# Optimization experiments

Hardware: AMD Instinct MI355X
Metric: run time of the kernel (lower is better)

Reference implementation:

```python
import jax, jax.numpy as jnp
import numpy as np

N_NODES = 50000
N_EDGES = 800000
N_GRAPHS = 64
IN_DIM, HID, OUT = 128, 128, 16


def gcn_conv(x, src, dst, deg_inv_sqrt, W, b):
    # x: [N, Cin]; src/dst: [E+N] (self-loops appended); W: [Cin, Cout]
    h = x @ W                                   # [N, Cout]
    norm = deg_inv_sqrt[src] * deg_inv_sqrt[dst]  # [E+N]
    msg = h[src] * norm[:, None]                # gather + scale
    out = jax.ops.segment_sum(msg, dst, num_segments=N_NODES)
    return out + b


def setup_inputs() -> dict:
    key = jax.random.key(0)
    ks = jax.random.split(key, 8)
    x = jax.random.normal(ks[0], (N_NODES, IN_DIM), dtype=jnp.float32)
    edge_index = jax.random.randint(ks[1], (2, N_EDGES), 0, N_NODES, dtype=jnp.int64)
    batch = jnp.sort(jax.random.randint(ks[2], (N_NODES,), 0, N_GRAPHS, dtype=jnp.int64))
    s = 1.0 / np.sqrt(IN_DIM)
    W1 = jax.random.normal(ks[3], (IN_DIM, HID), dtype=jnp.float32) * s
    b1 = jnp.zeros((HID,), dtype=jnp.float32)
    W2 = jax.random.normal(ks[4], (HID, HID), dtype=jnp.float32) * (1.0 / np.sqrt(HID))
    b2 = jnp.zeros((HID,), dtype=jnp.float32)
    Wfc = jax.random.normal(ks[5], (HID, OUT), dtype=jnp.float32) * (1.0 / np.sqrt(HID))
    bfc = jnp.zeros((OUT,), dtype=jnp.float32)
    return {"x": x, "edge_index": edge_index, "batch": batch,
            "W1": W1, "b1": b1, "W2": W2, "b2": b2, "Wfc": Wfc, "bfc": bfc}


def reference(x, edge_index, batch, W1, b1, W2, b2, Wfc, bfc):
    self_loops = jnp.arange(N_NODES, dtype=edge_index.dtype)
    src = jnp.concatenate([edge_index[0], self_loops])  # [E+N]
    dst = jnp.concatenate([edge_index[1], self_loops])
    deg = jax.ops.segment_sum(jnp.ones_like(dst, dtype=x.dtype), dst, num_segments=N_NODES)
    deg_inv_sqrt = jnp.where(deg > 0, jax.lax.rsqrt(deg), 0.0)

    h = jax.nn.relu(gcn_conv(x, src, dst, deg_inv_sqrt, W1, b1))
    h = jax.nn.relu(gcn_conv(h, src, dst, deg_inv_sqrt, W2, b2))

    # global mean pool over graphs
    sums = jax.ops.segment_sum(h, batch, num_segments=N_GRAPHS)         # [G, HID]
    cnts = jax.ops.segment_sum(jnp.ones((N_NODES,), h.dtype), batch, num_segments=N_GRAPHS)
    pooled = sums / jnp.maximum(cnts, 1.0)[:, None]

    return pooled @ Wfc + bfc  # [G, OUT]
```

## Files before the change

kernel.cpp:

```cpp
#include <hip/hip_runtime.h>
#include <math.h>

#define N_NODES 50000
#define N_EDGES 800000
#define N_GRAPHS 64
#define DIM 128
#define OUTD 16
#define POOL_BLOCKS 1024

#define BSHIFT 8
#define BNODES 256
#define NBUCK ((N_NODES + BNODES - 1) / BNODES)
#define TILE 2048
#define RCAP 8192
#define BSLOT 4864

typedef __attribute__((ext_vector_type(8))) short short8;
typedef __attribute__((ext_vector_type(4))) float f32x4;

static __device__ __forceinline__ unsigned short f2bf(float f) {
    unsigned u = __float_as_uint(f);
    u += 0x7fffu + ((u >> 16) & 1u);
    return (unsigned short)(u >> 16);
}
static __device__ __forceinline__ float bfl(unsigned u) {
    return __uint_as_float(u << 16);
}
static __device__ __forceinline__ float bfh(unsigned u) {
    return __uint_as_float(u & 0xffff0000u);
}
static __device__ __forceinline__ float b2f(unsigned short u) {
    return __uint_as_float((unsigned)u << 16);
}

__global__ __launch_bounds__(256) void k_init(int* __restrict__ cursor,
                                              float* __restrict__ pool,
                                              float* __restrict__ pcnt) {
    int tid = threadIdx.x;
    if (tid < NBUCK) cursor[tid] = tid * BSLOT;
    for (int i = tid; i < N_GRAPHS * DIM; i += 256) pool[i] = 0.f;
    if (tid < N_GRAPHS) pcnt[tid] = 0.f;
}

__global__ __launch_bounds__(256) void k_binA(const int* __restrict__ src,
                                              const int* __restrict__ dstp,
                                              int* __restrict__ bucket_cursor,
                                              unsigned* __restrict__ bucket_arr) {
    __shared__ int cnt[NBUCK];
    __shared__ int base[NBUCK];
    int tile0 = blockIdx.x * TILE;
    for (int i = threadIdx.x; i < NBUCK; i += 256) cnt[i] = 0;
    __syncthreads();
#pragma unroll
    for (int j = 0; j < TILE / 512; ++j) {
        int e = tile0 + j * 512 + threadIdx.x * 2;
        if (e < N_EDGES) {
            int2 d = *(const int2*)(dstp + e);
            atomicAdd(&cnt[d.x >> BSHIFT], 1);
            atomicAdd(&cnt[d.y >> BSHIFT], 1);
        }
    }
    __syncthreads();
    for (int i = threadIdx.x; i < NBUCK; i += 256) {
        int c = cnt[i];
        base[i] = c ? atomicAdd(&bucket_cursor[i], c) : 0;
        cnt[i] = 0;
    }
    __syncthreads();
#pragma unroll
    for (int j = 0; j < TILE / 512; ++j) {
        int e = tile0 + j * 512 + threadIdx.x * 2;
        if (e < N_EDGES) {
            int2 s = *(const int2*)(src + e);
            int2 d = *(const int2*)(dstp + e);
            int b0 = d.x >> BSHIFT, b1 = d.y >> BSHIFT;
            int p0 = base[b0] + atomicAdd(&cnt[b0], 1);
            bucket_arr[p0] = (unsigned)s.x | ((unsigned)(d.x & 255) << 16);
            int p1 = base[b1] + atomicAdd(&cnt[b1], 1);
            bucket_arr[p1] = (unsigned)s.y | ((unsigned)(d.y & 255) << 16);
        }
    }
}

__global__ __launch_bounds__(256) void k_bases(const int* __restrict__ cursor,
                                               int* __restrict__ base) {
    __shared__ int s[256];
    int tid = threadIdx.x;
    int v = (tid < NBUCK) ? (cursor[tid] - tid * BSLOT) : 0;
    s[tid] = v;
    __syncthreads();
    for (int off = 1; off < 256; off <<= 1) {
        int t = (tid >= off) ? s[tid - off] : 0;
        __syncthreads();
        s[tid] += t;
        __syncthreads();
    }
    if (tid <= NBUCK) base[tid] = s[tid] - v;
}

__global__ __launch_bounds__(256) void k_binB(const unsigned* __restrict__ barr,
                                              const int* __restrict__ base,
                                              int* __restrict__ row_off,
                                              float* __restrict__ dis,
                                              unsigned short* __restrict__ csr) {
    __shared__ unsigned raw[RCAP];
    __shared__ unsigned short stage[RCAP];
    __shared__ int hist[BNODES];
    __shared__ int scn[BNODES];
    int tid = threadIdx.x;
    int b = blockIdx.x;
    int n0 = b << BSHIFT;
    int rbase = base[b];
    int len = base[b + 1] - rbase;
    const unsigned* bin = barr + (size_t)b * BSLOT;

    hist[tid] = 0;
    __syncthreads();
    for (int i = tid; i < len; i += 256) {
        unsigned ed = bin[i];
        if (i < RCAP) raw[i] = ed;
        atomicAdd(&hist[ed >> 16], 1);
    }
    __syncthreads();
    int v = hist[tid];
    scn[tid] = v;
    __syncthreads();
    for (int off = 1; off < 256; off <<= 1) {
        int t = (tid >= off) ? scn[tid - off] : 0;
        __syncthreads();
        scn[tid] += t;
        __syncthreads();
    }
    int excl = scn[tid] - v;
    int n = n0 + tid;
    if (n < N_NODES) {
        row_off[n] = rbase + excl;
        dis[n] = rsqrtf((float)(v + 1));
    }
    if (b == NBUCK - 1 && tid == 0) row_off[N_NODES] = N_EDGES;
    hist[tid] = excl;
    __syncthreads();
    for (int i = tid; i < len; i += 256) {
        unsigned ed = (i < RCAP) ? raw[i] : bin[i];
        int p = atomicAdd(&hist[ed >> 16], 1);
        unsigned short sv = (unsigned short)(ed & 0xffffu);
        if (p < RCAP) stage[p] = sv;
        else csr[rbase + p] = sv;
    }
    __syncthreads();
    int lim = min(len, RCAP);
    for (int i = tid; i < lim; i += 256)
        csr[rbase + i] = stage[i];
}

template <int BF16IN>
__global__ __launch_bounds__(256) void k_gemm(const void* __restrict__ Av,
                                              const float* __restrict__ Wg,
                                              unsigned short* __restrict__ C,
                                              int nrows) {
    __shared__ unsigned smemW[32768 / 4];
    __shared__ unsigned smemC[34816 / 4];
    unsigned* Wl = smemW;
    {
        int t = threadIdx.x;
        int p = t & 63;
        int kp = p * 2;
        int n0 = (t >> 6) * 32;
        int kstep = kp >> 5;
        int quad = (kp >> 3) & 3;
        int jw = (kp & 7) >> 1;
        const float* r0 = Wg + (size_t)kp * DIM;
        const float* r1 = r0 + DIM;
        int rot = (p >> 2) & 7;
#pragma unroll
        for (int i4 = 0; i4 < 8; ++i4) {
            int nb = ((i4 + rot) & 7) * 4;
            int n = n0 + nb;
            float4 lo = *(const float4*)(r0 + n);
            float4 hi = *(const float4*)(r1 + n);
            const float* lp = &lo.x;
            const float* hp = &hi.x;
#pragma unroll
            for (int ii = 0; ii < 4; ++ii) {
                int nn = n + ii;
                int ct = nn >> 4;
                int l  = quad * 16 + (nn & 15);
                unsigned vlo = f2bf(lp[ii]);
                unsigned vhi = f2bf(hp[ii]);
                Wl[(((kstep * 8 + ct) * 64) + l) * 4 + jw] = vlo | (vhi << 16);
            }
        }
    }
    __syncthreads();

    int wid  = threadIdx.x >> 6;
    int lane = threadIdx.x & 63;
    int m    = lane & 15;
    int quad = lane >> 4;
    const short8* Wf = (const short8*)Wl;
    unsigned short* cs = (unsigned short*)smemC + wid * 4352;
    const unsigned char* cb = (const unsigned char*)smemC + wid * 8704;

    int ntiles = (nrows + 127) / 128;
    for (int tile = blockIdx.x; tile < ntiles; tile += gridDim.x) {
        int row0 = tile * 128 + wid * 32;
        if (row0 >= nrows) continue;

        int rA = row0 + m;      if (rA >= nrows) rA = nrows - 1;
        int rB = row0 + 16 + m; if (rB >= nrows) rB = nrows - 1;

        short8 af0[4], af1[4];
        if (BF16IN) {
            const unsigned short* arowA = (const unsigned short*)Av + (size_t)rA * DIM + quad * 8;
            const unsigned short* arowB = (const unsigned short*)Av + (size_t)rB * DIM + quad * 8;
#pragma unroll
            for (int ks = 0; ks < 4; ++ks) {
                af0[ks] = *(const short8*)(arowA + ks * 32);
                af1[ks] = *(const short8*)(arowB + ks * 32);
            }
        } else {
            const float* arowA = (const float*)Av + (size_t)rA * DIM + quad * 8;
            const float* arowB = (const float*)Av + (size_t)rB * DIM + quad * 8;
#pragma unroll
            for (int ks = 0; ks < 4; ++ks) {
                float4 lo = *(const float4*)(arowA + ks * 32);
                float4 hi = *(const float4*)(arowA + ks * 32 + 4);
                short8 f;
                f[0] = (short)f2bf(lo.x); f[1] = (short)f2bf(lo.y);
                f[2] = (short)f2bf(lo.z); f[3] = (short)f2bf(lo.w);
                f[4] = (short)f2bf(hi.x); f[5] = (short)f2bf(hi.y);
                f[6] = (short)f2bf(hi.z); f[7] = (short)f2bf(hi.w);
                af0[ks] = f;
                lo = *(const float4*)(arowB + ks * 32);
                hi = *(const float4*)(arowB + ks * 32 + 4);
                f[0] = (short)f2bf(lo.x); f[1] = (short)f2bf(lo.y);
                f[2] = (short)f2bf(lo.z); f[3] = (short)f2bf(lo.w);
                f[4] = (short)f2bf(hi.x); f[5] = (short)f2bf(hi.y);
                f[6] = (short)f2bf(hi.z); f[7] = (short)f2bf(hi.w);
                af1[ks] = f;
            }
        }

        f32x4 acc0[8], acc1[8];
#pragma unroll
        for (int ct = 0; ct < 8; ++ct) {
            acc0[ct] = (f32x4){0.f, 0.f, 0.f, 0.f};
            acc1[ct] = (f32x4){0.f, 0.f, 0.f, 0.f};
        }

#pragma unroll
        for (int ks = 0; ks < 4; ++ks) {
#pragma unroll
            for (int ct = 0; ct < 8; ++ct) {
                short8 bfrag = Wf[(ks * 8 + ct) * 64 + lane];
                acc0[ct] = __builtin_amdgcn_mfma_f32_16x16x32_bf16(af0[ks], bfrag, acc0[ct], 0, 0, 0);
                acc1[ct] = __builtin_amdgcn_mfma_f32_16x16x32_bf16(af1[ks], bfrag, acc1[ct], 0, 0, 0);
            }
        }

#pragma unroll
        for (int ct = 0; ct < 8; ++ct) {
#pragma unroll
            for (int reg = 0; reg < 4; ++reg) {
                cs[(quad * 4 + reg) * 136 + ct * 16 + m]      = f2bf(acc0[ct][reg]);
                cs[(16 + quad * 4 + reg) * 136 + ct * 16 + m] = f2bf(acc1[ct][reg]);
            }
        }
#pragma unroll
        for (int i = 0; i < 8; ++i) {
            int rg = i * 4 + quad;
            int r = row0 + rg;
            if (r < nrows) {
                uint4 vv = *(const uint4*)(cb + rg * 272 + m * 16);
                *((uint4*)(C + (size_t)r * DIM) + m) = vv;
            }
        }
    }
}

__global__ __launch_bounds__(256) void k_agg(const uint4* __restrict__ Hb4,
                                             const int* __restrict__ row_off,
                                             const unsigned short* __restrict__ csr,
                                             const float* __restrict__ dis,
                                             const float* __restrict__ bias,
                                             uint4* __restrict__ out) {
    int lane = threadIdx.x & 15;
    int node = blockIdx.x * 16 + (threadIdx.x >> 4);
    if (node >= N_NODES) return;

    float dn = dis[node];
    float wself = dn * dn;
    uint4 hp = Hb4[(size_t)node * 16 + lane];
    float a0[8], a1[8], a2[8], a3[8];
    a0[0] = wself * bfl(hp.x); a0[1] = wself * bfh(hp.x);
    a0[2] = wself * bfl(hp.y); a0[3] = wself * bfh(hp.y);
    a0[4] = wself * bfl(hp.z); a0[5] = wself * bfh(hp.z);
    a0[6] = wself * bfl(hp.w); a0[7] = wself * bfh(hp.w);
#pragma unroll
    for (int j = 0; j < 8; ++j) { a1[j] = 0.f; a2[j] = 0.f; a3[j] = 0.f; }

    int e = row_off[node], e1 = row_off[node + 1];
    for (; e + 4 <= e1; e += 4) {
        int s0 = csr[e];     int s1 = csr[e + 1];
        int s2 = csr[e + 2]; int s3 = csr[e + 3];
        uint4 g0 = Hb4[(size_t)s0 * 16 + lane];
        uint4 g1 = Hb4[(size_t)s1 * 16 + lane];
        uint4 g2 = Hb4[(size_t)s2 * 16 + lane];
        uint4 g3 = Hb4[(size_t)s3 * 16 + lane];
        float w0 = dn * dis[s0], w1 = dn * dis[s1];
        float w2 = dn * dis[s2], w3 = dn * dis[s3];
        a0[0] = fmaf(w0, bfl(g0.x), a0[0]); a0[1] = fmaf(w0, bfh(g0.x), a0[1]);
        a0[2] = fmaf(w0, bfl(g0.y), a0[2]); a0[3] = fmaf(w0, bfh(g0.y), a0[3]);
        a0[4] = fmaf(w0, bfl(g0.z), a0[4]); a0[5] = fmaf(w0, bfh(g0.z), a0[5]);
        a0[6] = fmaf(w0, bfl(g0.w), a0[6]); a0[7] = fmaf(w0, bfh(g0.w), a0[7]);
        a1[0] = fmaf(w1, bfl(g1.x), a1[0]); a1[1] = fmaf(w1, bfh(g1.x), a1[1]);
        a1[2] = fmaf(w1, bfl(g1.y), a1[2]); a1[3] = fmaf(w1, bfh(g1.y), a1[3]);
        a1[4] = fmaf(w1, bfl(g1.z), a1[4]); a1[5] = fmaf(w1, bfh(g1.z), a1[5]);
        a1[6] = fmaf(w1, bfl(g1.w), a1[6]); a1[7] = fmaf(w1, bfh(g1.w), a1[7]);
        a2[0] = fmaf(w2, bfl(g2.x), a2[0]); a2[1] = fmaf(w2, bfh(g2.x), a2[1]);
        a2[2] = fmaf(w2, bfl(g2.y), a2[2]); a2[3] = fmaf(w2, bfh(g2.y), a2[3]);
        a2[4] = fmaf(w2, bfl(g2.z), a2[4]); a2[5] = fmaf(w2, bfh(g2.z), a2[5]);
        a2[6] = fmaf(w2, bfl(g2.w), a2[6]); a2[7] = fmaf(w2, bfh(g2.w), a2[7]);
        a3[0] = fmaf(w3, bfl(g3.x), a3[0]); a3[1] = fmaf(w3, bfh(g3.x), a3[1]);
        a3[2] = fmaf(w3, bfl(g3.y), a3[2]); a3[3] = fmaf(w3, bfh(g3.y), a3[3]);
        a3[4] = fmaf(w3, bfl(g3.z), a3[4]); a3[5] = fmaf(w3, bfh(g3.z), a3[5]);
        a3[6] = fmaf(w3, bfl(g3.w), a3[6]); a3[7] = fmaf(w3, bfh(g3.w), a3[7]);
    }
    for (; e < e1; ++e) {
        int s = csr[e];
        uint4 g = Hb4[(size_t)s * 16 + lane];
        float w = dn * dis[s];
        a0[0] = fmaf(w, bfl(g.x), a0[0]); a0[1] = fmaf(w, bfh(g.x), a0[1]);
        a0[2] = fmaf(w, bfl(g.y), a0[2]); a0[3] = fmaf(w, bfh(g.y), a0[3]);
        a0[4] = fmaf(w, bfl(g.z), a0[4]); a0[5] = fmaf(w, bfh(g.z), a0[5]);
        a0[6] = fmaf(w, bfl(g.w), a0[6]); a0[7] = fmaf(w, bfh(g.w), a0[7]);
    }

    float4 b0 = ((const float4*)bias)[lane * 2];
    float4 b1v = ((const float4*)bias)[lane * 2 + 1];
    float r[8];
    r[0] = fmaxf(a0[0] + a1[0] + a2[0] + a3[0] + b0.x, 0.f);
    r[1] = fmaxf(a0[1] + a1[1] + a2[1] + a3[1] + b0.y, 0.f);
    r[2] = fmaxf(a0[2] + a1[2] + a2[2] + a3[2] + b0.z, 0.f);
    r[3] = fmaxf(a0[3] + a1[3] + a2[3] + a3[3] + b0.w, 0.f);
    r[4] = fmaxf(a0[4] + a1[4] + a2[4] + a3[4] + b1v.x, 0.f);
    r[5] = fmaxf(a0[5] + a1[5] + a2[5] + a3[5] + b1v.y, 0.f);
    r[6] = fmaxf(a0[6] + a1[6] + a2[6] + a3[6] + b1v.z, 0.f);
    r[7] = fmaxf(a0[7] + a1[7] + a2[7] + a3[7] + b1v.w, 0.f);
    uint4 ov;
    ov.x = (unsigned)f2bf(r[0]) | ((unsigned)f2bf(r[1]) << 16);
    ov.y = (unsigned)f2bf(r[2]) | ((unsigned)f2bf(r[3]) << 16);
    ov.z = (unsigned)f2bf(r[4]) | ((unsigned)f2bf(r[5]) << 16);
    ov.w = (unsigned)f2bf(r[6]) | ((unsigned)f2bf(r[7]) << 16);
    out[(size_t)node * 16 + lane] = ov;
}

__global__ __launch_bounds__(128) void k_pool(const unsigned short* __restrict__ h,
                                              const int* __restrict__ batch,
                                              float* __restrict__ pool,
                                              float* __restrict__ pcnt) {
    int chunk = (N_NODES + POOL_BLOCKS - 1) / POOL_BLOCKS;
    int n0 = blockIdx.x * chunk;
    int n1 = min(n0 + chunk, N_NODES);
    if (n0 >= n1) return;
    int c = threadIdx.x;
    int curg = batch[n0];
    float acc = 0.f;
    int count = 0;
    int n = n0;
    for (; n + 4 <= n1; ) {
        int g0 = batch[n], g3 = batch[n + 3];
        if (g0 == curg && g3 == curg) {
            float v0 = b2f(h[(size_t)(n + 0) * DIM + c]);
            float v1 = b2f(h[(size_t)(n + 1) * DIM + c]);
            float v2 = b2f(h[(size_t)(n + 2) * DIM + c]);
            float v3 = b2f(h[(size_t)(n + 3) * DIM + c]);
            acc += (v0 + v1) + (v2 + v3);
            count += 4;
            n += 4;
        } else {
            int g = g0;
            if (g != curg) {
                atomicAdd(&pool[curg * DIM + c], acc);
                if (c == 0) atomicAdd(&pcnt[curg], (float)count);
                acc = 0.f; count = 0; curg = g;
            }
            acc += b2f(h[(size_t)n * DIM + c]);
            count++;
            n += 1;
        }
    }
    for (; n < n1; ++n) {
        int g = batch[n];
        if (g != curg) {
            atomicAdd(&pool[curg * DIM + c], acc);
            if (c == 0) atomicAdd(&pcnt[curg], (float)count);
            acc = 0.f; count = 0; curg = g;
        }
        acc += b2f(h[(size_t)n * DIM + c]);
        count++;
    }
    atomicAdd(&pool[curg * DIM + c], acc);
    if (c == 0) atomicAdd(&pcnt[curg], (float)count);
}

__global__ void k_fc(const float* __restrict__ pool, const float* __restrict__ pcnt,
                     const float* __restrict__ Wfc, const float* __restrict__ bfc,
                     float* __restrict__ out) {
    int id = blockIdx.x * blockDim.x + threadIdx.x;
    if (id >= N_GRAPHS * OUTD) return;
    int g = id >> 4, o = id & 15;
    float inv = 1.0f / fmaxf(pcnt[g], 1.0f);
    float acc = bfc[o];
    const float* p = pool + g * DIM;
    for (int c = 0; c < DIM; ++c)
        acc = fmaf(p[c] * inv, Wfc[c * OUTD + o], acc);
    out[id] = acc;
}


extern "C" void kernel_launch(void* const* d_in, const int* in_sizes, int n_in,
                              void* d_out, int out_size, void* d_ws, size_t ws_size,
                              hipStream_t stream) {
    const float* x    = (const float*)d_in[0];
    const int*   ei   = (const int*)d_in[1];
    const int*   batch= (const int*)d_in[2];
    const float* W1   = (const float*)d_in[3];
    const float* b1   = (const float*)d_in[4];
    const float* W2   = (const float*)d_in[5];
    const float* b2   = (const float*)d_in[6];
    const float* Wfc  = (const float*)d_in[7];
    const float* bfc  = (const float*)d_in[8];
    float* out = (float*)d_out;

    char* ws = (char*)d_ws;
    size_t off = 0;
    auto alloc = [&](size_t bytes) -> char* {
        char* p = ws + off;
        off = (off + bytes + 255) & ~(size_t)255;
        return p;
    };
    int*      bbase    = (int*)     alloc((size_t)(NBUCK + 1) * 4);
    int*      bcursor  = (int*)     alloc((size_t)NBUCK * 4);
    int*      row_off  = (int*)     alloc((size_t)(N_NODES + 1) * 4);
    float*    dis      = (float*)   alloc((size_t)N_NODES * 4);
    unsigned short* csr= (unsigned short*)alloc((size_t)N_EDGES * 2);
    unsigned* barr     = (unsigned*)alloc((size_t)NBUCK * BSLOT * 4);
    float*    pool     = (float*)   alloc((size_t)N_GRAPHS * DIM * 4);
    float*    pcnt     = (float*)   alloc((size_t)N_GRAPHS * 4);
    unsigned short* Hb = (unsigned short*)alloc((size_t)N_NODES * DIM * 2);
    unsigned short* Hb2= (unsigned short*)alloc((size_t)N_NODES * DIM * 2);

    const int* src = ei;
    const int* dst = ei + N_EDGES;

    int bin_grid = (N_EDGES + TILE - 1) / TILE;
    k_init<<<1, 256, 0, stream>>>(bcursor, pool, pcnt);
    k_binA<<<bin_grid, 256, 0, stream>>>(src, dst, bcursor, barr);
    k_bases<<<1, 256, 0, stream>>>(bcursor, bbase);
    k_binB<<<NBUCK, 256, 0, stream>>>(barr, bbase, row_off, dis, csr);

    int agg_grid = (N_NODES + 15) / 16;
    k_gemm<0><<<256, 256, 0, stream>>>(x, W1, Hb, N_NODES);
    k_agg<<<agg_grid, 256, 0, stream>>>((const uint4*)Hb, row_off, csr, dis, b1, (uint4*)Hb2);
    k_gemm<1><<<256, 256, 0, stream>>>(Hb2, W2, Hb, N_NODES);
    k_agg<<<agg_grid, 256, 0, stream>>>((const uint4*)Hb, row_off, csr, dis, b2, (uint4*)Hb2);
    k_pool<<<POOL_BLOCKS, DIM, 0, stream>>>(Hb2, batch, pool, pcnt);
    k_fc<<<(N_GRAPHS * OUTD + 255) / 256, 256, 0, stream>>>(pool, pcnt, Wfc, bfc, out);
}
```

Measured before the change: 219.5 us.

## Fuse edge binning into first GEMM launch and fold bucket-base scan into binB

Merges the edge-bucketing pass (binA) and the first GEMM into one launch, where blocks beyond the GEMM count do binning, so the two independent stages can overlap. The separate k_bases scan kernel is removed: bucket counts are kept directly and each binB block redoes the small prefix scan over bucket counts itself. This cuts two kernel launches and their serialization gaps. In exchange, every binB block does a redundant 256-entry scan, and the fused kernel's shared memory footprint applies to the binning blocks too, which may lower their occupancy.

After: 207.9 us. 1.06x faster.

```diff
diff --git a/kernel.cpp b/kernel.cpp
--- a/kernel.cpp
+++ b/kernel.cpp
@@ -14,6 +14,8 @@
 #define TILE 2048
 #define RCAP 8192
 #define BSLOT 4864
+#define GEMMB 256
+#define BIN_GRID ((N_EDGES + TILE - 1) / TILE)
 
 typedef __attribute__((ext_vector_type(8))) short short8;
 typedef __attribute__((ext_vector_type(4))) float f32x4;
@@ -33,133 +35,22 @@
     return __uint_as_float((unsigned)u << 16);
 }
 
-__global__ __launch_bounds__(256) void k_init(int* __restrict__ cursor,
+__global__ __launch_bounds__(256) void k_init(int* __restrict__ bcnt,
                                               float* __restrict__ pool,
                                               float* __restrict__ pcnt) {
     int tid = threadIdx.x;
-    if (tid < NBUCK) cursor[tid] = tid * BSLOT;
+    if (tid < NBUCK) bcnt[tid] = 0;
     for (int i = tid; i < N_GRAPHS * DIM; i += 256) pool[i] = 0.f;
     if (tid < N_GRAPHS) pcnt[tid] = 0.f;
 }
 
-__global__ __launch_bounds__(256) void k_binA(const int* __restrict__ src,
-                                              const int* __restrict__ dstp,
-                                              int* __restrict__ bucket_cursor,
-                                              unsigned* __restrict__ bucket_arr) {
-    __shared__ int cnt[NBUCK];
-    __shared__ int base[NBUCK];
-    int tile0 = blockIdx.x * TILE;
-    for (int i = threadIdx.x; i < NBUCK; i += 256) cnt[i] = 0;
-    __syncthreads();
-#pragma unroll
-    for (int j = 0; j < TILE / 512; ++j) {
-        int e = tile0 + j * 512 + threadIdx.x * 2;
-        if (e < N_EDGES) {
-            int2 d = *(const int2*)(dstp + e);
-            atomicAdd(&cnt[d.x >> BSHIFT], 1);
-            atomicAdd(&cnt[d.y >> BSHIFT], 1);
-        }
-    }
-    __syncthreads();
-    for (int i = threadIdx.x; i < NBUCK; i += 256) {
-        int c = cnt[i];
-        base[i] = c ? atomicAdd(&bucket_cursor[i], c) : 0;
-        cnt[i] = 0;
-    }
-    __syncthreads();
-#pragma unroll
-    for (int j = 0; j < TILE / 512; ++j) {
-        int e = tile0 + j * 512 + threadIdx.x * 2;
-        if (e < N_EDGES) {
-            int2 s = *(const int2*)(src + e);
-            int2 d = *(const int2*)(dstp + e);
-            int b0 = d.x >> BSHIFT, b1 = d.y >> BSHIFT;
-            int p0 = base[b0] + atomicAdd(&cnt[b0], 1);
-            bucket_arr[p0] = (unsigned)s.x | ((unsigned)(d.x & 255) << 16);
-            int p1 = base[b1] + atomicAdd(&cnt[b1], 1);
-            bucket_arr[p1] = (unsigned)s.y | ((unsigned)(d.y & 255) << 16);
-        }
-    }
-}
-
-__global__ __launch_bounds__(256) void k_bases(const int* __restrict__ cursor,
-                                               int* __restrict__ base) {
-    __shared__ int s[256];
-    int tid = threadIdx.x;
-    int v = (tid < NBUCK) ? (cursor[tid] - tid * BSLOT) : 0;
-    s[tid] = v;
-    __syncthreads();
-    for (int off = 1; off < 256; off <<= 1) {
-        int t = (tid >= off) ? s[tid - off] : 0;
-        __syncthreads();
-        s[tid] += t;
-        __syncthreads();
-    }
-    if (tid <= NBUCK) base[tid] = s[tid] - v;
-}
-
-__global__ __launch_bounds__(256) void k_binB(const unsigned* __restrict__ barr,
-                                              const int* __restrict__ base,
-                                              int* __restrict__ row_off,
-                                              float* __restrict__ dis,
-                                              unsigned short* __restrict__ csr) {
-    __shared__ unsigned raw[RCAP];
-    __shared__ unsigned short stage[RCAP];
-    __shared__ int hist[BNODES];
-    __shared__ int scn[BNODES];
-    int tid = threadIdx.x;
-    int b = blockIdx.x;
-    int n0 = b << BSHIFT;
-    int rbase = base[b];
-    int len = base[b + 1] - rbase;
-    const unsigned* bin = barr + (size_t)b * BSLOT;
-
-    hist[tid] = 0;
-    __syncthreads();
-    for (int i = tid; i < len; i += 256) {
-        unsigned ed = bin[i];
-        if (i < RCAP) raw[i] = ed;
-        atomicAdd(&hist[ed >> 16], 1);
-    }
-    __syncthreads();
-    int v = hist[tid];
-    scn[tid] = v;
-    __syncthreads();
-    for (int off = 1; off < 256; off <<= 1) {
-        int t = (tid >= off) ? scn[tid - off] : 0;
-        __syncthreads();
-        scn[tid] += t;
-        __syncthreads();
-    }
-    int excl = scn[tid] - v;
-    int n = n0 + tid;
-    if (n < N_NODES) {
-        row_off[n] = rbase + excl;
-        dis[n] = rsqrtf((float)(v + 1));
-    }
-    if (b == NBUCK - 1 && tid == 0) row_off[N_NODES] = N_EDGES;
-    hist[tid] = excl;
-    __syncthreads();
-    for (int i = tid; i < len; i += 256) {
-        unsigned ed = (i < RCAP) ? raw[i] : bin[i];
-        int p = atomicAdd(&hist[ed >> 16], 1);
-        unsigned short sv = (unsigned short)(ed & 0xffffu);
-        if (p < RCAP) stage[p] = sv;
-        else csr[rbase + p] = sv;
-    }
-    __syncthreads();
-    int lim = min(len, RCAP);
-    for (int i = tid; i < lim; i += 256)
-        csr[rbase + i] = stage[i];
-}
-
 template <int BF16IN>
-__global__ __launch_bounds__(256) void k_gemm(const void* __restrict__ Av,
-                                              const float* __restrict__ Wg,
-                                              unsigned short* __restrict__ C,
-                                              int nrows) {
-    __shared__ unsigned smemW[32768 / 4];
-    __shared__ unsigned smemC[34816 / 4];
+static __device__ __forceinline__ void gemm_body(const void* __restrict__ Av,
+                                                 const float* __restrict__ Wg,
+                                                 unsigned short* __restrict__ C,
+                                                 int nrows,
+                                                 unsigned* smemW, unsigned* smemC,
+                                                 int tile0, int tstride) {
     unsigned* Wl = smemW;
     {
         int t = threadIdx.x;
@@ -202,7 +93,7 @@
     const unsigned char* cb = (const unsigned char*)smemC + wid * 8704;
 
     int ntiles = (nrows + 127) / 128;
-    for (int tile = blockIdx.x; tile < ntiles; tile += gridDim.x) {
+    for (int tile = tile0; tile < ntiles; tile += tstride) {
         int row0 = tile * 128 + wid * 32;
         if (row0 >= nrows) continue;
 
@@ -276,6 +167,132 @@
             }
         }
     }
+}
+
+__global__ __launch_bounds__(256) void k_fused1(const float* __restrict__ A,
+                                                const float* __restrict__ Wg,
+                                                unsigned short* __restrict__ C,
+                                                int nrows,
+                                                const int* __restrict__ src,
+                                                const int* __restrict__ dstp,
+                                                int* __restrict__ bcnt,
+                                                unsigned* __restrict__ bucket_arr) {
+    __shared__ unsigned smemW[32768 / 4];
+    __shared__ unsigned smemC[34816 / 4];
+    if (blockIdx.x >= GEMMB) {
+        int* cnt  = (int*)smemW;
+        int* base = cnt + NBUCK;
+        int tile0 = (blockIdx.x - GEMMB) * TILE;
+        for (int i = threadIdx.x; i < NBUCK; i += 256) cnt[i] = 0;
+        __syncthreads();
+#pragma unroll
+        for (int j = 0; j < TILE / 512; ++j) {
+            int e = tile0 + j * 512 + threadIdx.x * 2;
+            if (e < N_EDGES) {
+                int2 d = *(const int2*)(dstp + e);
+                atomicAdd(&cnt[d.x >> BSHIFT], 1);
+                atomicAdd(&cnt[d.y >> BSHIFT], 1);
+            }
+        }
+        __syncthreads();
+        for (int i = threadIdx.x; i < NBUCK; i += 256) {
+            int c = cnt[i];
+            base[i] = i * BSLOT + (c ? atomicAdd(&bcnt[i], c) : 0);
+            cnt[i] = 0;
+        }
+        __syncthreads();
+#pragma unroll
+        for (int j = 0; j < TILE / 512; ++j) {
+            int e = tile0 + j * 512 + threadIdx.x * 2;
+            if (e < N_EDGES) {
+                int2 s = *(const int2*)(src + e);
+                int2 d = *(const int2*)(dstp + e);
+                int b0 = d.x >> BSHIFT, b1 = d.y >> BSHIFT;
+                int p0 = base[b0] + atomicAdd(&cnt[b0], 1);
+                bucket_arr[p0] = (unsigned)s.x | ((unsigned)(d.x & 255) << 16);
+                int p1 = base[b1] + atomicAdd(&cnt[b1], 1);
+                bucket_arr[p1] = (unsigned)s.y | ((unsigned)(d.y & 255) << 16);
+            }
+        }
+        return;
+    }
+    gemm_body<0>(A, Wg, C, nrows, smemW, smemC, blockIdx.x, GEMMB);
+}
+
+__global__ __launch_bounds__(256) void k_gemm2(const unsigned short* __restrict__ A,
+                                               const float* __restrict__ Wg,
+                                               unsigned short* __restrict__ C,
+                                               int nrows) {
+    __shared__ unsigned smemW[32768 / 4];
+    __shared__ unsigned smemC[34816 / 4];
+    gemm_body<1>(A, Wg, C, nrows, smemW, smemC, blockIdx.x, gridDim.x);
+}
+
+__global__ __launch_bounds__(256) void k_binB(const unsigned* __restrict__ barr,
+                                              const int* __restrict__ bcnt,
+                                              int* __restrict__ row_off,
+                                              float* __restrict__ dis,
+                                              unsigned short* __restrict__ csr) {
+    __shared__ unsigned raw[RCAP];
+    __shared__ unsigned short stage[RCAP];
+    __shared__ int hist[BNODES];
+    __shared__ int scn[BNODES];
+    __shared__ int borig[256], bscan[256];
+    int tid = threadIdx.x;
+    int b = blockIdx.x;
+    int n0 = b << BSHIFT;
+
+    int cv = (tid < NBUCK) ? bcnt[tid] : 0;
+    borig[tid] = cv;
+    bscan[tid] = cv;
+    __syncthreads();
+    for (int off = 1; off < 256; off <<= 1) {
+        int t = (tid >= off) ? bscan[tid - off] : 0;
+        __syncthreads();
+        bscan[tid] += t;
+        __syncthreads();
+    }
+    int rbase = bscan[b] - borig[b];
+    int len = borig[b];
+    const unsigned* bin = barr + (size_t)b * BSLOT;
+
+    hist[tid] = 0;
+    __syncthreads();
+    for (int i = tid; i < len; i += 256) {
+        unsigned ed = bin[i];
+        if (i < RCAP) raw[i] = ed;
+        atomicAdd(&hist[ed >> 16], 1);
+    }
+    __syncthreads();
+    int v = hist[tid];
+    scn[tid] = v;
+    __syncthreads();
+    for (int off = 1; off < 256; off <<= 1) {
+        int t = (tid >= off) ? scn[tid - off] : 0;
+        __syncthreads();
+        scn[tid] += t;
+        __syncthreads();
+    }
+    int excl = scn[tid] - v;
+    int n = n0 + tid;
+    if (n < N_NODES) {
+        row_off[n] = rbase + excl;
+        dis[n] = rsqrtf((float)(v + 1));
+    }
+    if (b == NBUCK - 1 && tid == 0) row_off[N_NODES] = N_EDGES;
+    hist[tid] = excl;
+    __syncthreads();
+    for (int i = tid; i < len; i += 256) {
+        unsigned ed = (i < RCAP) ? raw[i] : bin[i];
+        int p = atomicAdd(&hist[ed >> 16], 1);
+        unsigned short sv = (unsigned short)(ed & 0xffffu);
+        if (p < RCAP) stage[p] = sv;
+        else csr[rbase + p] = sv;
+    }
+    __syncthreads();
+    int lim = min(len, RCAP);
+    for (int i = tid; i < lim; i += 256)
+        csr[rbase + i] = stage[i];
 }
 
 __global__ __launch_bounds__(256) void k_agg(const uint4* __restrict__ Hb4,
@@ -440,8 +457,7 @@
         off = (off + bytes + 255) & ~(size_t)255;
         return p;
     };
-    int*      bbase    = (int*)     alloc((size_t)(NBUCK + 1) * 4);
-    int*      bcursor  = (int*)     alloc((size_t)NBUCK * 4);
+    int*      bcnt     = (int*)     alloc((size_t)NBUCK * 4);
     int*      row_off  = (int*)     alloc((size_t)(N_NODES + 1) * 4);
     float*    dis      = (float*)   alloc((size_t)N_NODES * 4);
     unsigned short* csr= (unsigned short*)alloc((size_t)N_EDGES * 2);
@@ -454,16 +470,14 @@
     const int* src = ei;
     const int* dst = ei + N_EDGES;
 
-    int bin_grid = (N_EDGES + TILE - 1) / TILE;
-    k_init<<<1, 256, 0, stream>>>(bcursor, pool, pcnt);
-    k_binA<<<bin_grid, 256, 0, stream>>>(src, dst, bcursor, barr);
-    k_bases<<<1, 256, 0, stream>>>(bcursor, bbase);
-    k_binB<<<NBUCK, 256, 0, stream>>>(barr, bbase, row_off, dis, csr);
+    k_init<<<1, 256, 0, stream>>>(bcnt, pool, pcnt);
+    k_fused1<<<GEMMB + BIN_GRID, 256, 0, stream>>>(x, W1, Hb, N_NODES,
+                                                   src, dst, bcnt, barr);
+    k_binB<<<NBUCK, 256, 0, stream>>>(barr, bcnt, row_off, dis, csr);
 
     int agg_grid = (N_NODES + 15) / 16;
-    k_gemm<0><<<256, 256, 0, stream>>>(x, W1, Hb, N_NODES);
     k_agg<<<agg_grid, 256, 0, stream>>>((const uint4*)Hb, row_off, csr, dis, b1, (uint4*)Hb2);
-    k_gemm<1><<<256, 256, 0, stream>>>(Hb2, W2, Hb, N_NODES);
+    k_gemm2<<<GEMMB, 256, 0, stream>>>(Hb2, W2, Hb, N_NODES);
     k_agg<<<agg_grid, 256, 0, stream>>>((const uint4*)Hb, row_off, csr, dis, b2, (uint4*)Hb2);
     k_pool<<<POOL_BLOCKS, DIM, 0, stream>>>(Hb2, batch, pool, pcnt);
     k_fc<<<(N_GRAPHS * OUTD + 255) / 256, 256, 0, stream>>>(pool, pcnt, Wfc, bfc, out);
```
